# Kernel tuning notes

Hardware: AMD Instinct MI355X
Metric: run time of the kernel (lower is better)

The kernel has to match this reference:

```python
import jax, jax.numpy as jnp
import numpy as np

HEADS = 4
DIM_HEAD = 32
DIM = 128
EPS = 1e-5


def layer_norm(x, g, b):
    m = jnp.mean(x, axis=-1, keepdims=True)
    v = jnp.var(x, axis=-1, keepdims=True)
    return (x - m) * jax.lax.rsqrt(v + EPS) * g + b


def setup_inputs() -> dict:
    key = jax.random.key(0)
    ks = jax.random.split(key, 24)
    B, D, Hb, Wb = 1, DIM, 50, 50
    N, h, w = 6, 24, 44
    Q = Hb * Wb
    NK = N * h * w
    inner = HEADS * DIM_HEAD
    s = 0.02
    inp = {
        'q': jax.random.normal(ks[0], (B, D, Hb, Wb), jnp.float32),
        'k': jax.random.normal(ks[1], (B, N, D, h, w), jnp.float32),
        'v': jax.random.normal(ks[2], (B, N, D, h, w), jnp.float32),
        'W_logits': jax.random.uniform(ks[3], (B, Q, NK), jnp.float32),
        'vis': jax.random.randint(ks[4], (B, Q, NK), 0, 2, jnp.int32),
        'skip': jax.random.normal(ks[5], (B, D, Hb, Wb), jnp.float32),
        'qn_g': jnp.ones((D,)), 'qn_b': jnp.zeros((D,)),
        'kn_g': jnp.ones((D,)), 'kn_b': jnp.zeros((D,)),
        'vn_g': jnp.ones((D,)), 'vn_b': jnp.zeros((D,)),
        'wq': s * jax.random.normal(ks[6], (inner, D)), 'bq': jnp.zeros((inner,)),
        'wk': s * jax.random.normal(ks[7], (inner, D)), 'bk': jnp.zeros((inner,)),
        'wv': s * jax.random.normal(ks[8], (inner, D)), 'bv': jnp.zeros((inner,)),
        'wproj': s * jax.random.normal(ks[9], (D, inner)), 'bproj': jnp.zeros((D,)),
        'pre_g': jnp.ones((D,)), 'pre_b': jnp.zeros((D,)),
        'w1': s * jax.random.normal(ks[10], (2 * D, D)), 'b1': jnp.zeros((2 * D,)),
        'w2': s * jax.random.normal(ks[11], (D, 2 * D)), 'b2': jnp.zeros((D,)),
        'post_g': jnp.ones((D,)), 'post_b': jnp.zeros((D,)),
    }
    return inp


def reference(q, k, v, W_logits, vis, skip,
              qn_g, qn_b, kn_g, kn_b, vn_g, vn_b,
              wq, bq, wk, bk, wv, bv, wproj, bproj,
              pre_g, pre_b, w1, b1, w2, b2, post_g, post_b):
    B, D, Hb, Wb = q.shape
    Q = Hb * Wb
    scale = DIM_HEAD ** (-0.5)
    # flatten: q -> [B, Q, D]; k,v [B,N,D,h,w] -> [B, NK, D]
    qf = q.reshape(B, D, Q).transpose(0, 2, 1)
    kf = jnp.transpose(k, (0, 1, 3, 4, 2)).reshape(B, -1, D)
    vf = jnp.transpose(v, (0, 1, 3, 4, 2)).reshape(B, -1, D)
    qf = layer_norm(qf, qn_g, qn_b) @ wq.T + bq
    kf = layer_norm(kf, kn_g, kn_b) @ wk.T + bk
    vf = layer_norm(vf, vn_g, vn_b) @ wv.T + bv
    # split heads -> [B, H, Q/K, dh]
    qh = qf.reshape(B, Q, HEADS, DIM_HEAD).transpose(0, 2, 1, 3)
    kh = kf.reshape(B, -1, HEADS, DIM_HEAD).transpose(0, 2, 1, 3)
    vh = vf.reshape(B, -1, HEADS, DIM_HEAD).transpose(0, 2, 1, 3)
    logits = jnp.einsum('bhqd,bhkd->bhqk', qh, kh) * scale
    neg_inf = jnp.finfo(logits.dtype).min
    logits = jnp.where(vis[:, None] == 0, neg_inf, logits)
    logits = logits * W_logits[:, None]
    attn = jax.nn.softmax(logits, axis=-1)
    out = jnp.einsum('bhqk,bhkd->bhqd', attn, vh)
    out = out.transpose(0, 2, 1, 3).reshape(B, Q, HEADS * DIM_HEAD)
    out = out @ wproj.T + bproj
    z = out.transpose(0, 2, 1).reshape(B, D, Hb, Wb) + skip
    zf = z.reshape(B, D, Q).transpose(0, 2, 1)
    zf = layer_norm(zf, pre_g, pre_b)
    hmid = jax.nn.gelu(zf @ w1.T + b1, approximate=False)
    zf = zf + (hmid @ w2.T + b2)
    zf = layer_norm(zf, post_g, post_b)
    return zf.transpose(0, 2, 1).reshape(B, D, Hb, Wb)
```

## Files before the change

### kernel.cpp

```cpp
#include <hip/hip_runtime.h>
#include <hip/hip_bf16.h>

typedef __attribute__((ext_vector_type(8))) short bf16x8;
typedef __attribute__((ext_vector_type(4))) float f32x4;

#define NQ 2500
#define NKK 6336
#define NHEADS 4
#define DHEAD 32
#define CSC 0.25503482f
#define BIGNEG (-1.0e30f)

#define WS_QP 0
#define WS_KP 640000
#define WS_VT 2262016
#define WS_WB 3884032
#define WS_OP 4146176
#define OSPLIT_F 340000
#define OROW_F 136
#define WS_REQ3 8226176ULL
#define WS_REQ4 9586176ULL
#define WS_REQ6 12306176ULL

#define WQB 0
#define WKB 16384
#define WVB 32768
#define WPROJB 49152
#define W1B 65536
#define W2B 98304

#define NTILES_TOTAL 99
#define TQ 16
#define ATQ 32
#define TK 64
#define QBLOCKS 157
#define AQBLOCKS 79

#define KSTR 136
#define VSTR 72
#define PSTR 72
#define ABSTR 68

__device__ __forceinline__ unsigned short bf16bits(float x) {
  union { __hip_bfloat16 h; unsigned short s; } cv;
  cv.h = __float2bfloat16(x);
  return cv.s;
}

__global__ __launch_bounds__(256) void wconv_kernel(
    const float* __restrict__ wq, const float* __restrict__ wk,
    const float* __restrict__ wv, const float* __restrict__ wproj,
    const float* __restrict__ w1, const float* __restrict__ w2,
    __hip_bfloat16* __restrict__ wb)
{
  int e = (blockIdx.x * 256 + threadIdx.x) * 4;
  const float* src; int off;
  if (e < 16384)      { src = wq;    off = e; }
  else if (e < 32768) { src = wk;    off = e - 16384; }
  else if (e < 49152) { src = wv;    off = e - 32768; }
  else if (e < 65536) { src = wproj; off = e - 49152; }
  else if (e < 98304) { src = w1;    off = e - 65536; }
  else                { src = w2;    off = e - 98304; }
  float4 v = *(const float4*)(src + off);
  ushort4 o4;
  o4.x = bf16bits(v.x); o4.y = bf16bits(v.y); o4.z = bf16bits(v.z); o4.w = bf16bits(v.w);
  *(ushort4*)((unsigned short*)wb + e) = o4;
}

__global__ __launch_bounds__(256) void lnproj_kernel(
    const float* __restrict__ qin, const float* __restrict__ kin, const float* __restrict__ vin,
    const float* __restrict__ qn_g, const float* __restrict__ qn_b,
    const float* __restrict__ kn_g, const float* __restrict__ kn_b,
    const float* __restrict__ vn_g, const float* __restrict__ vn_b,
    const __hip_bfloat16* __restrict__ wball,
    const float* __restrict__ bq, const float* __restrict__ bk, const float* __restrict__ bv,
    __hip_bfloat16* __restrict__ Qp, __hip_bfloat16* __restrict__ Kp,
    __hip_bfloat16* __restrict__ Vt)
{
  __shared__ __hip_bfloat16 lxb[32][136];
  __shared__ float lpart[32][8][2];
  __shared__ float lmr[32][2];
  __shared__ float lgb[128], lbeb[128];

  const int t = threadIdx.x;
  const int bb = blockIdx.x;
  int mode, row0;
  const float *in, *g, *be, *bo;
  const __hip_bfloat16* wb;
  if (bb < 79)       { mode = 0; row0 = bb * 32;         in = qin; g = qn_g; be = qn_b; wb = wball + WQB; bo = bq; }
  else if (bb < 277) { mode = 1; row0 = (bb - 79) * 32;  in = kin; g = kn_g; be = kn_b; wb = wball + WKB; bo = bk; }
  else               { mode = 2; row0 = (bb - 277) * 32; in = vin; g = vn_g; be = vn_b; wb = wball + WVB; bo = bv; }

  if (t < 128) { lgb[t] = g[t]; lbeb[t] = be[t]; }

  const int row = t & 31, seg = t >> 5;
  int grow = row0 + row;
  size_t base, dstr;
  bool rvalid = true;
  if (mode == 0) { rvalid = (grow < NQ); base = (size_t)(rvalid ? grow : NQ - 1); dstr = NQ; }
  else { int n = grow / 1056, rr = grow - n * 1056; base = (size_t)n * 135168 + rr; dstr = 1056; }

  float xr[16];
  float s = 0.f, ss = 0.f;
  #pragma unroll
  for (int i = 0; i < 16; ++i) {
    float x = in[base + (size_t)(seg * 16 + i) * dstr];
    xr[i] = x; s += x; ss += x * x;
  }
  lpart[row][seg][0] = s; lpart[row][seg][1] = ss;
  __syncthreads();
  if (t < 32) {
    float S = 0.f, SS = 0.f;
    #pragma unroll
    for (int j = 0; j < 8; ++j) { S += lpart[t][j][0]; SS += lpart[t][j][1]; }
    float mean = S * (1.f / 128.f);
    float var  = SS * (1.f / 128.f) - mean * mean;
    lmr[t][0] = mean;
    lmr[t][1] = rsqrtf(fmaxf(var, 0.f) + 1e-5f);
  }
  __syncthreads();
  {
    float mean = lmr[row][0], rstd = lmr[row][1];
    #pragma unroll
    for (int i = 0; i < 16; ++i) {
      int d = seg * 16 + i;
      lxb[row][d] = __float2bfloat16((xr[i] - mean) * rstd * lgb[d] + lbeb[d]);
    }
  }
  __syncthreads();

  const int wid = t >> 6, lane = t & 63;
  const int n16 = lane & 15, quad = lane >> 4;
  const int ow = wid * 32;

  f32x4 acc[2][2] = {};
  for (int kt = 0; kt < 4; ++kt) {
    bf16x8 af[2];
    #pragma unroll
    for (int mi = 0; mi < 2; ++mi)
      af[mi] = *(const bf16x8*)&lxb[mi * 16 + n16][kt * 32 + quad * 8];
    #pragma unroll
    for (int ni = 0; ni < 2; ++ni) {
      bf16x8 bw = *(const bf16x8*)(wb + (size_t)(ow + ni * 16 + n16) * 128 + kt * 32 + quad * 8);
      #pragma unroll
      for (int mi = 0; mi < 2; ++mi)
        acc[mi][ni] = __builtin_amdgcn_mfma_f32_16x16x32_bf16(af[mi], bw, acc[mi][ni], 0, 0, 0);
    }
  }

  float bias[2];
  #pragma unroll
  for (int ni = 0; ni < 2; ++ni) bias[ni] = bo[ow + ni * 16 + n16];

  #pragma unroll
  for (int mi = 0; mi < 2; ++mi) {
    int gr0 = row0 + mi * 16 + quad * 4;
    if (mode == 2) {
      #pragma unroll
      for (int ni = 0; ni < 2; ++ni) {
        int o = ow + ni * 16 + n16;
        ushort4 v4;
        v4.x = bf16bits(acc[mi][ni][0] + bias[ni]);
        v4.y = bf16bits(acc[mi][ni][1] + bias[ni]);
        v4.z = bf16bits(acc[mi][ni][2] + bias[ni]);
        v4.w = bf16bits(acc[mi][ni][3] + bias[ni]);
        *(ushort4*)((unsigned short*)Vt + (size_t)o * NKK + gr0) = v4;
      }
    } else {
      #pragma unroll
      for (int rg = 0; rg < 4; ++rg) {
        int gr = gr0 + rg;
        if (mode != 0 || gr < NQ) {
          #pragma unroll
          for (int ni = 0; ni < 2; ++ni) {
            int o = ow + ni * 16 + n16;
            __hip_bfloat16 b16 = __float2bfloat16(acc[mi][ni][rg] + bias[ni]);
            if (mode == 0) Qp[(size_t)gr * 128 + o] = b16;
            else           Kp[(size_t)gr * 128 + o] = b16;
          }
        }
      }
    }
  }
}

__global__ __launch_bounds__(256, 2) void attn_kernel(
    const __hip_bfloat16* __restrict__ Qp,
    const __hip_bfloat16* __restrict__ Kp,
    const __hip_bfloat16* __restrict__ Vt,
    const float* __restrict__ Wl,
    const int* __restrict__ vis,
    float* __restrict__ Opart)
{
  __shared__ alignas(16) __hip_bfloat16 lk[TK * KSTR];
  __shared__ alignas(16) __hip_bfloat16 lv[128 * VSTR];
  __shared__ alignas(16) float sc[ATQ * ABSTR];
  __shared__ alignas(16) __hip_bfloat16 lp[NHEADS * ATQ * PSTR];

  const int t = threadIdx.x;
  const int lane = t & 63;
  const int h = t >> 6;
  const int n16 = lane & 15;
  const int quad = lane >> 4;
  const int q0 = blockIdx.x * ATQ;
  const int split = blockIdx.y;
  const int ksplit = gridDim.y;
  const int tstart = (NTILES_TOTAL * split) / ksplit;
  const int ntiles = (NTILES_TOTAL * (split + 1)) / ksplit - tstart;

  bf16x8 aq[2];
  #pragma unroll
  for (int m = 0; m < 2; ++m) {
    int gqa = q0 + m * 16 + n16; if (gqa >= NQ) gqa = NQ - 1;
    aq[m] = *(const bf16x8*)(Qp + (size_t)gqa * 128 + h * DHEAD + quad * 8);
  }

  const int kr = t >> 2, kc = (t & 3) * 32;
  const int vr = t >> 1, vc = (t & 1) * 32;
  const int qq = t >> 3, kkc = (t & 7) * 8;
  int gqe = q0 + qq; if (gqe >= NQ) gqe = NQ - 1;
  const size_t wbase = (size_t)gqe * NKK + kkc;

  bf16x8 bones;
  {
    short one = (short)0x3F80;
    short val = (n16 == 0) ? one : (short)0;
    #pragma unroll
    for (int j = 0; j < 8; ++j) bones[j] = val;
  }

  uint4 pk0, pk1, pk2, pk3, pv0, pv1, pv2, pv3;
  float4 pw0, pw1; int4 pvs0, pvs1;

  auto issue = [&](int tile) {
    int k0 = (tstart + tile) * TK;
    const uint4* ksrc = (const uint4*)(Kp + (size_t)(k0 + kr) * 128 + kc);
    pk0 = ksrc[0]; pk1 = ksrc[1]; pk2 = ksrc[2]; pk3 = ksrc[3];
    const uint4* vsrc = (const uint4*)(Vt + (size_t)vr * NKK + k0 + vc);
    pv0 = vsrc[0]; pv1 = vsrc[1]; pv2 = vsrc[2]; pv3 = vsrc[3];
    pw0  = *(const float4*)(Wl + wbase + k0);
    pw1  = *(const float4*)(Wl + wbase + k0 + 4);
    pvs0 = *(const int4*)(vis + wbase + k0);
    pvs1 = *(const int4*)(vis + wbase + k0 + 4);
  };
  auto commit = [&]() {
    uint4* kd = (uint4*)&lk[kr * KSTR + kc];
    kd[0] = pk0; kd[1] = pk1; kd[2] = pk2; kd[3] = pk3;
    uint4* vd = (uint4*)&lv[vr * VSTR + vc];
    vd[0] = pv0; vd[1] = pv1; vd[2] = pv2; vd[3] = pv3;
    float4 c0, c1;
    c0.x = pvs0.x ? pw0.x * CSC : BIGNEG * pw0.x;
    c0.y = pvs0.y ? pw0.y * CSC : BIGNEG * pw0.y;
    c0.z = pvs0.z ? pw0.z * CSC : BIGNEG * pw0.z;
    c0.w = pvs0.w ? pw0.w * CSC : BIGNEG * pw0.w;
    c1.x = pvs1.x ? pw1.x * CSC : BIGNEG * pw1.x;
    c1.y = pvs1.y ? pw1.y * CSC : BIGNEG * pw1.y;
    c1.z = pvs1.z ? pw1.z * CSC : BIGNEG * pw1.z;
    c1.w = pvs1.w ? pw1.w * CSC : BIGNEG * pw1.w;
    *(float4*)&sc[qq * ABSTR + kkc] = c0;
    *(float4*)&sc[qq * ABSTR + kkc + 4] = c1;
  };

  f32x4 o[2][3];
  #pragma unroll
  for (int m = 0; m < 2; ++m)
    #pragma unroll
    for (int j = 0; j < 3; ++j)
      o[m][j] = f32x4{0.f, 0.f, 0.f, 0.f};

  issue(0);
  commit();
  __syncthreads();

  for (int kt = 0; kt < ntiles; ++kt) {
    if (kt + 1 < ntiles) issue(kt + 1);

    f32x4 s[2][4];
    #pragma unroll
    for (int ks = 0; ks < 4; ++ks) {
      bf16x8 bk = *(const bf16x8*)&lk[(ks * 16 + n16) * KSTR + h * DHEAD + quad * 8];
      f32x4 z = {0.f, 0.f, 0.f, 0.f};
      s[0][ks] = __builtin_amdgcn_mfma_f32_16x16x32_bf16(aq[0], bk, z, 0, 0, 0);
      s[1][ks] = __builtin_amdgcn_mfma_f32_16x16x32_bf16(aq[1], bk, z, 0, 0, 0);
    }
    #pragma unroll
    for (int m = 0; m < 2; ++m) {
      #pragma unroll
      for (int ks = 0; ks < 4; ++ks) {
        #pragma unroll
        for (int r = 0; r < 4; ++r) {
          int row = m * 16 + quad * 4 + r;
          float c = sc[row * ABSTR + ks * 16 + n16];
          float tt = s[m][ks][r] * c;
          float arg = (c >= 0.f) ? tt : c;
          float p = exp2f(fminf(arg, 60.f));
          lp[h * (ATQ * PSTR) + row * PSTR + ks * 16 + n16] = __float2bfloat16(p);
        }
      }
    }
    #pragma unroll
    for (int kk = 0; kk < 2; ++kk) {
      bf16x8 bv0 = *(const bf16x8*)&lv[(h * DHEAD + n16) * VSTR + kk * 32 + quad * 8];
      bf16x8 bv1 = *(const bf16x8*)&lv[(h * DHEAD + 16 + n16) * VSTR + kk * 32 + quad * 8];
      #pragma unroll
      for (int m = 0; m < 2; ++m) {
        bf16x8 ap = *(const bf16x8*)&lp[h * (ATQ * PSTR) + (m * 16 + n16) * PSTR + kk * 32 + quad * 8];
        o[m][0] = __builtin_amdgcn_mfma_f32_16x16x32_bf16(ap, bv0, o[m][0], 0, 0, 0);
        o[m][1] = __builtin_amdgcn_mfma_f32_16x16x32_bf16(ap, bv1, o[m][1], 0, 0, 0);
        o[m][2] = __builtin_amdgcn_mfma_f32_16x16x32_bf16(ap, bones, o[m][2], 0, 0, 0);
      }
    }

    if (kt + 1 < ntiles) {
      __syncthreads();
      commit();
      __syncthreads();
    }
  }

  #pragma unroll
  for (int m = 0; m < 2; ++m) {
    #pragma unroll
    for (int r = 0; r < 4; ++r) {
      int gq = q0 + m * 16 + quad * 4 + r;
      if (gq < NQ) {
        float* rowp = Opart + (size_t)split * OSPLIT_F + (size_t)gq * OROW_F;
        rowp[h * DHEAD + n16] = o[m][0][r];
        rowp[h * DHEAD + 16 + n16] = o[m][1][r];
        if (n16 == 0) rowp[128 + h] = o[m][2][r];
      }
    }
  }
}

__global__ __launch_bounds__(256) void mlp_kernel(
    const float* __restrict__ Opart, int ksplit,
    const float* __restrict__ skip,
    const __hip_bfloat16* __restrict__ wball,
    const float* __restrict__ bproj,
    const float* __restrict__ pre_g, const float* __restrict__ pre_b,
    const float* __restrict__ b1, const float* __restrict__ b2,
    const float* __restrict__ post_g, const float* __restrict__ post_b,
    float* __restrict__ out)
{
  __shared__ __hip_bfloat16 sab[16][136];
  __shared__ __hip_bfloat16 znb[16][136];
  __shared__ float znf[16][132];
  __shared__ __hip_bfloat16 hb[16][264];
  __shared__ float part[16][4][2];

  const __hip_bfloat16* wprojb = wball + WPROJB;
  const __hip_bfloat16* w1b    = wball + W1B;
  const __hip_bfloat16* w2b    = wball + W2B;

  const int t = threadIdx.x;
  const int q0 = blockIdx.x * TQ;

  {
    int row = t >> 4, c0 = (t & 15) * 8;
    int gq = q0 + row; int cq = gq < NQ ? gq : NQ - 1;
    int head = c0 >> 5;
    float ll = 0.f;
    float acc8[8] = {};
    for (int s = 0; s < ksplit; ++s) {
      const float* rp = Opart + (size_t)s * OSPLIT_F + (size_t)cq * OROW_F;
      ll += rp[128 + head];
      float4 a = *(const float4*)(rp + c0);
      float4 b = *(const float4*)(rp + c0 + 4);
      acc8[0] += a.x; acc8[1] += a.y; acc8[2] += a.z; acc8[3] += a.w;
      acc8[4] += b.x; acc8[5] += b.y; acc8[6] += b.z; acc8[7] += b.w;
    }
    float rll = 1.f / fmaxf(ll, 1e-30f);
    #pragma unroll
    for (int i = 0; i < 8; ++i)
      sab[row][c0 + i] = __float2bfloat16(acc8[i] * rll);
  }
  __syncthreads();

  const int wid = t >> 6, lane = t & 63;
  const int n16 = lane & 15, quad = lane >> 4;
  const int qrow0 = q0 + quad * 4;

  f32x4 acc1[2] = {};
  for (int kt = 0; kt < 4; ++kt) {
    bf16x8 af = *(const bf16x8*)&sab[n16][kt * 32 + quad * 8];
    #pragma unroll
    for (int ni = 0; ni < 2; ++ni) {
      int o = wid * 32 + ni * 16 + n16;
      bf16x8 bw = *(const bf16x8*)(wprojb + (size_t)o * 128 + kt * 32 + quad * 8);
      acc1[ni] = __builtin_amdgcn_mfma_f32_16x16x32_bf16(af, bw, acc1[ni], 0, 0, 0);
    }
  }
  float z[2][4];
  #pragma unroll
  for (int ni = 0; ni < 2; ++ni) {
    int o = wid * 32 + ni * 16 + n16;
    float bo = bproj[o];
    if (qrow0 + 3 < NQ) {
      float4 sk = *(const float4*)(skip + (size_t)o * NQ + qrow0);
      z[ni][0] = acc1[ni][0] + bo + sk.x;
      z[ni][1] = acc1[ni][1] + bo + sk.y;
      z[ni][2] = acc1[ni][2] + bo + sk.z;
      z[ni][3] = acc1[ni][3] + bo + sk.w;
    } else {
      #pragma unroll
      for (int rg = 0; rg < 4; ++rg) {
        int cq = qrow0 + rg < NQ ? qrow0 + rg : NQ - 1;
        z[ni][rg] = acc1[ni][rg] + bo + skip[(size_t)o * NQ + cq];
      }
    }
  }
  #pragma unroll
  for (int rg = 0; rg < 4; ++rg) {
    float s = z[0][rg] + z[1][rg];
    float ss = z[0][rg] * z[0][rg] + z[1][rg] * z[1][rg];
    s += __shfl_xor(s, 1);  ss += __shfl_xor(ss, 1);
    s += __shfl_xor(s, 2);  ss += __shfl_xor(ss, 2);
    s += __shfl_xor(s, 4);  ss += __shfl_xor(ss, 4);
    s += __shfl_xor(s, 8);  ss += __shfl_xor(ss, 8);
    if (n16 == 0) { part[quad * 4 + rg][wid][0] = s; part[quad * 4 + rg][wid][1] = ss; }
  }
  __syncthreads();
  #pragma unroll
  for (int rg = 0; rg < 4; ++rg) {
    int row = quad * 4 + rg;
    float S  = part[row][0][0] + part[row][1][0] + part[row][2][0] + part[row][3][0];
    float SS = part[row][0][1] + part[row][1][1] + part[row][2][1] + part[row][3][1];
    float mean = S * (1.f / 128.f);
    float var  = SS * (1.f / 128.f) - mean * mean;
    float rstd = rsqrtf(fmaxf(var, 0.f) + 1e-5f);
    #pragma unroll
    for (int ni = 0; ni < 2; ++ni) {
      int o = wid * 32 + ni * 16 + n16;
      float zn = (z[ni][rg] - mean) * rstd * pre_g[o] + pre_b[o];
      znf[row][o] = zn;
      znb[row][o] = __float2bfloat16(zn);
    }
  }
  __syncthreads();

  f32x4 acc2[4] = {};
  for (int kt = 0; kt < 4; ++kt) {
    bf16x8 af = *(const bf16x8*)&znb[n16][kt * 32 + quad * 8];
    #pragma unroll
    for (int ni = 0; ni < 4; ++ni) {
      int j = wid * 64 + ni * 16 + n16;
      bf16x8 bw = *(const bf16x8*)(w1b + (size_t)j * 128 + kt * 32 + quad * 8);
      acc2[ni] = __builtin_amdgcn_mfma_f32_16x16x32_bf16(af, bw, acc2[ni], 0, 0, 0);
    }
  }
  #pragma unroll
  for (int ni = 0; ni < 4; ++ni) {
    int j = wid * 64 + ni * 16 + n16;
    float bj = b1[j];
    #pragma unroll
    for (int rg = 0; rg < 4; ++rg) {
      float a1 = acc2[ni][rg] + bj;
      hb[quad * 4 + rg][j] = __float2bfloat16(0.5f * a1 * (1.0f + erff(a1 * 0.70710678118654752f)));
    }
  }
  __syncthreads();

  f32x4 acc3[2] = {};
  for (int kt = 0; kt < 8; ++kt) {
    bf16x8 af = *(const bf16x8*)&hb[n16][kt * 32 + quad * 8];
    #pragma unroll
    for (int ni = 0; ni < 2; ++ni) {
      int o = wid * 32 + ni * 16 + n16;
      bf16x8 bw = *(const bf16x8*)(w2b + (size_t)o * 256 + kt * 32 + quad * 8);
      acc3[ni] = __builtin_amdgcn_mfma_f32_16x16x32_bf16(af, bw, acc3[ni], 0, 0, 0);
    }
  }
  float y[2][4];
  #pragma unroll
  for (int ni = 0; ni < 2; ++ni) {
    int o = wid * 32 + ni * 16 + n16;
    float bo = b2[o];
    #pragma unroll
    for (int rg = 0; rg < 4; ++rg)
      y[ni][rg] = znf[quad * 4 + rg][o] + acc3[ni][rg] + bo;
  }
  #pragma unroll
  for (int rg = 0; rg < 4; ++rg) {
    float s = y[0][rg] + y[1][rg];
    float ss = y[0][rg] * y[0][rg] + y[1][rg] * y[1][rg];
    s += __shfl_xor(s, 1);  ss += __shfl_xor(ss, 1);
    s += __shfl_xor(s, 2);  ss += __shfl_xor(ss, 2);
    s += __shfl_xor(s, 4);  ss += __shfl_xor(ss, 4);
    s += __shfl_xor(s, 8);  ss += __shfl_xor(ss, 8);
    if (n16 == 0) { part[quad * 4 + rg][wid][0] = s; part[quad * 4 + rg][wid][1] = ss; }
  }
  __syncthreads();
  #pragma unroll
  for (int rg = 0; rg < 4; ++rg) {
    int row = quad * 4 + rg;
    float S  = part[row][0][0] + part[row][1][0] + part[row][2][0] + part[row][3][0];
    float SS = part[row][0][1] + part[row][1][1] + part[row][2][1] + part[row][3][1];
    float mean = S * (1.f / 128.f);
    float var  = SS * (1.f / 128.f) - mean * mean;
    float rstd = rsqrtf(fmaxf(var, 0.f) + 1e-5f);
    #pragma unroll
    for (int ni = 0; ni < 2; ++ni) {
      int o = wid * 32 + ni * 16 + n16;
      y[ni][rg] = (y[ni][rg] - mean) * rstd * post_g[o] + post_b[o];
    }
  }
  #pragma unroll
  for (int ni = 0; ni < 2; ++ni) {
    int o = wid * 32 + ni * 16 + n16;
    if (qrow0 + 3 < NQ) {
      *(float4*)(out + (size_t)o * NQ + qrow0) = make_float4(y[ni][0], y[ni][1], y[ni][2], y[ni][3]);
    } else {
      #pragma unroll
      for (int rg = 0; rg < 4; ++rg)
        if (qrow0 + rg < NQ) out[(size_t)o * NQ + qrow0 + rg] = y[ni][rg];
    }
  }
}

extern "C" void kernel_launch(void* const* d_in, const int* in_sizes, int n_in,
                              void* d_out, int out_size, void* d_ws, size_t ws_size,
                              hipStream_t stream) {
  if (ws_size < WS_REQ3) return;
  const int ksplit = (ws_size >= WS_REQ6) ? 6 : (ws_size >= WS_REQ4) ? 4 : 3;

  const float* q     = (const float*)d_in[0];
  const float* k     = (const float*)d_in[1];
  const float* v     = (const float*)d_in[2];
  const float* Wl    = (const float*)d_in[3];
  const int*   vis   = (const int*)d_in[4];
  const float* skip  = (const float*)d_in[5];
  const float* qn_g  = (const float*)d_in[6];
  const float* qn_b  = (const float*)d_in[7];
  const float* kn_g  = (const float*)d_in[8];
  const float* kn_b  = (const float*)d_in[9];
  const float* vn_g  = (const float*)d_in[10];
  const float* vn_b  = (const float*)d_in[11];
  const float* wq    = (const float*)d_in[12];
  const float* bq    = (const float*)d_in[13];
  const float* wk    = (const float*)d_in[14];
  const float* bk    = (const float*)d_in[15];
  const float* wv    = (const float*)d_in[16];
  const float* bv    = (const float*)d_in[17];
  const float* wproj = (const float*)d_in[18];
  const float* bproj = (const float*)d_in[19];
  const float* pre_g = (const float*)d_in[20];
  const float* pre_b = (const float*)d_in[21];
  const float* w1    = (const float*)d_in[22];
  const float* b1    = (const float*)d_in[23];
  const float* w2    = (const float*)d_in[24];
  const float* b2    = (const float*)d_in[25];
  const float* post_g= (const float*)d_in[26];
  const float* post_b= (const float*)d_in[27];

  char* ws = (char*)d_ws;
  __hip_bfloat16* Qp = (__hip_bfloat16*)(ws + WS_QP);
  __hip_bfloat16* Kp = (__hip_bfloat16*)(ws + WS_KP);
  __hip_bfloat16* Vt = (__hip_bfloat16*)(ws + WS_VT);
  __hip_bfloat16* Wb = (__hip_bfloat16*)(ws + WS_WB);
  float* Opart = (float*)(ws + WS_OP);

  hipLaunchKernelGGL(wconv_kernel, dim3(128), dim3(256), 0, stream,
                     wq, wk, wv, wproj, w1, w2, Wb);

  hipLaunchKernelGGL(lnproj_kernel, dim3(475), dim3(256), 0, stream,
                     q, k, v, qn_g, qn_b, kn_g, kn_b, vn_g, vn_b,
                     Wb, bq, bk, bv, Qp, Kp, Vt);

  hipLaunchKernelGGL(attn_kernel, dim3(AQBLOCKS, ksplit), dim3(256), 0, stream,
                     Qp, Kp, Vt, Wl, vis, Opart);

  hipLaunchKernelGGL(mlp_kernel, dim3(QBLOCKS), dim3(256), 0, stream,
                     Opart, ksplit, skip, Wb, bproj, pre_g, pre_b,
                     b1, b2, post_g, post_b, (float*)d_out);
}
```

Measured before the change: 249.2 us.

## Keep attention probabilities in registers via transposed QK MFMA and lane shuffles

The QK^T MFMA now takes swapped operands, so each lane holds transposed score fragments. The bf16 probabilities are packed in registers and redistributed with wave shuffles into the A-operand layout for the PV MFMA, which removes the shared-memory P buffer and its write/read round trip. The smaller LDS footprint allows raising launch bounds to 3 blocks per SM. A ksplit of 8 is also added when the workspace is large enough. In exchange there are more shuffle instructions and higher register pressure under the tighter occupancy bound.

```diff
diff --git a/kernel.cpp b/kernel.cpp
--- a/kernel.cpp
+++ b/kernel.cpp
@@ -21,6 +21,7 @@
 #define WS_REQ3 8226176ULL
 #define WS_REQ4 9586176ULL
 #define WS_REQ6 12306176ULL
+#define WS_REQ8 15026176ULL
 
 #define WQB 0
 #define WKB 16384
@@ -38,7 +39,6 @@
 
 #define KSTR 136
 #define VSTR 72
-#define PSTR 72
 #define ABSTR 68
 
 __device__ __forceinline__ unsigned short bf16bits(float x) {
@@ -184,7 +184,7 @@
   }
 }
 
-__global__ __launch_bounds__(256, 2) void attn_kernel(
+__global__ __launch_bounds__(256, 3) void attn_kernel(
     const __hip_bfloat16* __restrict__ Qp,
     const __hip_bfloat16* __restrict__ Kp,
     const __hip_bfloat16* __restrict__ Vt,
@@ -195,7 +195,6 @@
   __shared__ alignas(16) __hip_bfloat16 lk[TK * KSTR];
   __shared__ alignas(16) __hip_bfloat16 lv[128 * VSTR];
   __shared__ alignas(16) float sc[ATQ * ABSTR];
-  __shared__ alignas(16) __hip_bfloat16 lp[NHEADS * ATQ * PSTR];
 
   const int t = threadIdx.x;
   const int lane = t & 63;
@@ -220,6 +219,10 @@
   const int qq = t >> 3, kkc = (t & 7) * 8;
   int gqe = q0 + qq; if (gqe >= NQ) gqe = NQ - 1;
   const size_t wbase = (size_t)gqe * NKK + kkc;
+
+  const int shl0 = ((2 * quad) & 3) * 16 + n16;
+  const int shl1 = ((2 * quad + 1) & 3) * 16 + n16;
+  const bool hi = quad >= 2;
 
   bf16x8 bones;
   {
@@ -275,27 +278,32 @@
   for (int kt = 0; kt < ntiles; ++kt) {
     if (kt + 1 < ntiles) issue(kt + 1);
 
-    f32x4 s[2][4];
+    f32x4 st[2][4];
     #pragma unroll
     for (int ks = 0; ks < 4; ++ks) {
       bf16x8 bk = *(const bf16x8*)&lk[(ks * 16 + n16) * KSTR + h * DHEAD + quad * 8];
       f32x4 z = {0.f, 0.f, 0.f, 0.f};
-      s[0][ks] = __builtin_amdgcn_mfma_f32_16x16x32_bf16(aq[0], bk, z, 0, 0, 0);
-      s[1][ks] = __builtin_amdgcn_mfma_f32_16x16x32_bf16(aq[1], bk, z, 0, 0, 0);
-    }
+      st[0][ks] = __builtin_amdgcn_mfma_f32_16x16x32_bf16(bk, aq[0], z, 0, 0, 0);
+      st[1][ks] = __builtin_amdgcn_mfma_f32_16x16x32_bf16(bk, aq[1], z, 0, 0, 0);
+    }
+    unsigned pk[2][4][2];
     #pragma unroll
     for (int m = 0; m < 2; ++m) {
       #pragma unroll
       for (int ks = 0; ks < 4; ++ks) {
-        #pragma unroll
-        for (int r = 0; r < 4; ++r) {
-          int row = m * 16 + quad * 4 + r;
-          float c = sc[row * ABSTR + ks * 16 + n16];
-          float tt = s[m][ks][r] * c;
-          float arg = (c >= 0.f) ? tt : c;
-          float p = exp2f(fminf(arg, 60.f));
-          lp[h * (ATQ * PSTR) + row * PSTR + ks * 16 + n16] = __float2bfloat16(p);
+        float4 c4 = *(const float4*)&sc[(m * 16 + n16) * ABSTR + ks * 16 + quad * 4];
+        float p[4];
+        {
+          float cc[4] = {c4.x, c4.y, c4.z, c4.w};
+          #pragma unroll
+          for (int r = 0; r < 4; ++r) {
+            float tt = st[m][ks][r] * cc[r];
+            float arg = (cc[r] >= 0.f) ? tt : cc[r];
+            p[r] = exp2f(fminf(arg, 60.f));
+          }
         }
+        pk[m][ks][0] = (unsigned)bf16bits(p[0]) | ((unsigned)bf16bits(p[1]) << 16);
+        pk[m][ks][1] = (unsigned)bf16bits(p[2]) | ((unsigned)bf16bits(p[3]) << 16);
       }
     }
     #pragma unroll
@@ -304,10 +312,23 @@
       bf16x8 bv1 = *(const bf16x8*)&lv[(h * DHEAD + 16 + n16) * VSTR + kk * 32 + quad * 8];
       #pragma unroll
       for (int m = 0; m < 2; ++m) {
-        bf16x8 ap = *(const bf16x8*)&lp[h * (ATQ * PSTR) + (m * 16 + n16) * PSTR + kk * 32 + quad * 8];
-        o[m][0] = __builtin_amdgcn_mfma_f32_16x16x32_bf16(ap, bv0, o[m][0], 0, 0, 0);
-        o[m][1] = __builtin_amdgcn_mfma_f32_16x16x32_bf16(ap, bv1, o[m][1], 0, 0, 0);
-        o[m][2] = __builtin_amdgcn_mfma_f32_16x16x32_bf16(ap, bones, o[m][2], 0, 0, 0);
+        unsigned s00 = __shfl(pk[m][2 * kk][0], shl0);
+        unsigned s01 = __shfl(pk[m][2 * kk + 1][0], shl0);
+        unsigned r0 = hi ? s01 : s00;
+        unsigned s10 = __shfl(pk[m][2 * kk][1], shl0);
+        unsigned s11 = __shfl(pk[m][2 * kk + 1][1], shl0);
+        unsigned r1 = hi ? s11 : s10;
+        unsigned s20 = __shfl(pk[m][2 * kk][0], shl1);
+        unsigned s21 = __shfl(pk[m][2 * kk + 1][0], shl1);
+        unsigned r2 = hi ? s21 : s20;
+        unsigned s30 = __shfl(pk[m][2 * kk][1], shl1);
+        unsigned s31 = __shfl(pk[m][2 * kk + 1][1], shl1);
+        unsigned r3 = hi ? s31 : s30;
+        union { unsigned u[4]; bf16x8 v; } ap;
+        ap.u[0] = r0; ap.u[1] = r1; ap.u[2] = r2; ap.u[3] = r3;
+        o[m][0] = __builtin_amdgcn_mfma_f32_16x16x32_bf16(ap.v, bv0, o[m][0], 0, 0, 0);
+        o[m][1] = __builtin_amdgcn_mfma_f32_16x16x32_bf16(ap.v, bv1, o[m][1], 0, 0, 0);
+        o[m][2] = __builtin_amdgcn_mfma_f32_16x16x32_bf16(ap.v, bones, o[m][2], 0, 0, 0);
       }
     }
 
@@ -522,7 +543,9 @@
                               void* d_out, int out_size, void* d_ws, size_t ws_size,
                               hipStream_t stream) {
   if (ws_size < WS_REQ3) return;
-  const int ksplit = (ws_size >= WS_REQ6) ? 6 : (ws_size >= WS_REQ4) ? 4 : 3;
+  const int ksplit = (ws_size >= WS_REQ8) ? 8 :
+                     (ws_size >= WS_REQ6) ? 6 :
+                     (ws_size >= WS_REQ4) ? 4 : 3;
 
   const float* q     = (const float*)d_in[0];
   const float* k     = (const float*)d_in[1];
```

Measured after the change: 250.9 us. Within noise of the previous version (+0.7%).
